# Kernel optimization log

Measured on AMD Instinct MI355X. Metric: run time of the kernel, lower is better.

Reference implementation:

```python
import jax, jax.numpy as jnp
import numpy as np

V = 8192
E = 262144
IN_DIM = 128
OUT_DIM = 128
NEG_SLOPE = 0.2


def setup_inputs() -> dict:
    key = jax.random.key(0)
    k1, k2, k3, k4 = jax.random.split(key, 4)
    h = jax.random.normal(k1, (V, IN_DIM), dtype=jnp.float32)
    edge_index = jax.random.randint(k2, (2, E), 0, V, dtype=jnp.int64)
    # nn.Linear weights: W (out_dim, in_dim), att (1, 2*out_dim), both bias-free
    W = jax.random.normal(k3, (OUT_DIM, IN_DIM), dtype=jnp.float32) / np.sqrt(IN_DIM)
    att_w = jax.random.normal(k4, (1, 2 * OUT_DIM), dtype=jnp.float32) / np.sqrt(2 * OUT_DIM)
    return {"h": h, "edge_index": edge_index, "W": W, "att_w": att_w}


def reference(h, edge_index, W, att_w):
    # h: (V, in_dim) -> (V, out_dim)
    hw = h @ W.T
    src, dst = edge_index[0], edge_index[1]
    # edge features: concat of endpoint embeddings -> (E, 2*out_dim)
    e = jnp.concatenate([hw[src], hw[dst]], axis=-1)
    # attention logits per edge, LeakyReLU(0.2)
    a = jax.nn.leaky_relu(jnp.squeeze(e @ att_w.T, -1), negative_slope=NEG_SLOPE)
    v = hw.shape[0]
    # faithful to original: dense V x V matrix, zeros on non-edges,
    # softmax over ALL columns (non-edges included as score 0)
    alpha = jnp.zeros((v, v), dtype=hw.dtype).at[src, dst].set(a)
    alpha = jax.nn.softmax(alpha, axis=-1)
    # dropout is identity in eval mode (deterministic reference)
    return alpha @ hw
```

## Files before the change

### kernel.cpp

```cpp
#include <hip/hip_runtime.h>
#include <hip/hip_bf16.h>
#include <math.h>


#define V 8192
#define E 262144
#define D 128
#define NEG_SLOPE 0.2f
#define CAP 96

__global__ __launch_bounds__(256) void k_hw(const float* __restrict__ h,
                                            const float* __restrict__ W,
                                            const float* __restrict__ att,
                                            float* __restrict__ hw,
                                            float* __restrict__ s1,
                                            float* __restrict__ s2,
                                            float* __restrict__ S) {
    __shared__ float Wt[D * 132];
    __shared__ float hs[8][D];
    __shared__ float atts[2 * D];
    for (int e = threadIdx.x; e < D * D; e += 256) {
        int o = e >> 7, k = e & 127;
        Wt[k * 132 + o] = W[e];
    }
    atts[threadIdx.x] = att[threadIdx.x];
    int c4 = (threadIdx.x & 31) * 4;
    int rsel = threadIdx.x >> 5;
    int rowbase = blockIdx.x * 32;
    float4 cs = make_float4(0.f, 0.f, 0.f, 0.f);
    for (int it = 0; it < 4; ++it) {
        int r0 = rowbase + it * 8;
        __syncthreads();
        for (int e = threadIdx.x; e < 8 * D; e += 256)
            hs[e >> 7][e & 127] = h[(r0 + (e >> 7)) * D + (e & 127)];
        __syncthreads();
        float a0 = 0.f, a1 = 0.f, a2 = 0.f, a3 = 0.f;
        const float* hrow = hs[rsel];
        #pragma unroll 8
        for (int k = 0; k < D; ++k) {
            float hk = hrow[k];
            float4 wv = *(const float4*)&Wt[k * 132 + c4];
            a0 += hk * wv.x; a1 += hk * wv.y; a2 += hk * wv.z; a3 += hk * wv.w;
        }
        int row = r0 + rsel;
        *(float4*)&hw[row * D + c4] = make_float4(a0, a1, a2, a3);
        cs.x += a0; cs.y += a1; cs.z += a2; cs.w += a3;
        float p1 = a0 * atts[c4] + a1 * atts[c4 + 1] + a2 * atts[c4 + 2] + a3 * atts[c4 + 3];
        float p2 = a0 * atts[D + c4] + a1 * atts[D + c4 + 1] + a2 * atts[D + c4 + 2] + a3 * atts[D + c4 + 3];
        #pragma unroll
        for (int m = 16; m; m >>= 1) {
            p1 += __shfl_xor(p1, m);
            p2 += __shfl_xor(p2, m);
        }
        if ((threadIdx.x & 31) == 0) { s1[row] = p1; s2[row] = p2; }
    }
    __syncthreads();
    hs[rsel][c4] = cs.x; hs[rsel][c4 + 1] = cs.y; hs[rsel][c4 + 2] = cs.z; hs[rsel][c4 + 3] = cs.w;
    __syncthreads();
    if (threadIdx.x < D) {
        float t = 0.f;
        #pragma unroll
        for (int r = 0; r < 8; ++r) t += hs[r][threadIdx.x];
        atomicAdd(&S[threadIdx.x], t);
    }
}

__global__ __launch_bounds__(256) void k_scatter(const int* __restrict__ ei,
                                                 const float* __restrict__ s1,
                                                 const float* __restrict__ s2,
                                                 int* __restrict__ cnt,
                                                 int2* __restrict__ bucket) {
    int e = blockIdx.x * 256 + threadIdx.x;
    int src = ei[e];
    int dst = ei[E + e];
    float a = s1[src] + s2[dst];
    a = a > 0.f ? a : NEG_SLOPE * a;
    float w = expf(a) - 1.f;
    int pos = atomicAdd(&cnt[src], 1);
    if (pos < CAP)
        bucket[src * CAP + pos] = make_int2(dst, __float_as_int(w));
}

__global__ __launch_bounds__(256) void k_row(const int2* __restrict__ bucket,
                                             const int* __restrict__ cnt,
                                             const float* __restrict__ hw,
                                             const float* __restrict__ S,
                                             float* __restrict__ out) {
    int row = (blockIdx.x * 256 + threadIdx.x) >> 6;
    int lane = threadIdx.x & 63;
    int deg = cnt[row];
    if (deg > CAP) deg = CAP;
    const int2* b = bucket + row * CAP;
    int2 e0 = b[lane];
    int2 e1 = (lane < CAP - 64) ? b[64 + lane] : make_int2(-1, 0);
    int d0 = e0.x; float w0 = __int_as_float(e0.y);
    int d1 = e1.x; float w1 = __int_as_float(e1.y);
    if (lane >= deg)      { d0 = -1; w0 = 0.f; }
    if (64 + lane >= deg) { d1 = -1; w1 = 0.f; }
    float2 acc = make_float2(0.f, 0.f);
    float dex = 0.f;
    int dmax0 = deg < 64 ? deg : 64;
    for (int j = 0; j < dmax0; ++j) {
        int   dj = __shfl(d0, j);
        float wj = __shfl(w0, j);
        bool dup = (d0 == dj) && (lane < j);
        if (__any(dup)) continue;
        float2 hv = *(const float2*)&hw[dj * D + lane * 2];
        acc.x += wj * hv.x; acc.y += wj * hv.y;
        dex += wj;
    }
    for (int j = 64; j < deg; ++j) {
        int   dj = __shfl(d1, j - 64);
        float wj = __shfl(w1, j - 64);
        bool dup = (d0 == dj) || ((d1 == dj) && (64 + lane < j));
        if (__any(dup)) continue;
        float2 hv = *(const float2*)&hw[dj * D + lane * 2];
        acc.x += wj * hv.x; acc.y += wj * hv.y;
        dex += wj;
    }
    float inv = 1.f / ((float)V + dex);
    float2 s = *(const float2*)&S[lane * 2];
    float2 o;
    o.x = (s.x + acc.x) * inv;
    o.y = (s.y + acc.y) * inv;
    *(float2*)&out[row * D + lane * 2] = o;
}

extern "C" void kernel_launch(void* const* d_in, const int* in_sizes, int n_in,
                              void* d_out, int out_size, void* d_ws, size_t ws_size,
                              hipStream_t stream) {
    const float* h   = (const float*)d_in[0];
    const int*   ei  = (const int*)d_in[1];
    const float* W   = (const float*)d_in[2];
    const float* att = (const float*)d_in[3];
    float* out = (float*)d_out;

    char* ws = (char*)d_ws;
    float* hw  = (float*)(ws);
    float* s1  = (float*)(ws + 4194304);
    float* s2  = (float*)(ws + 4227072);
    float* S   = (float*)(ws + 4259840);
    int*   cnt = (int*)(ws + 4260352);
    int2*  bucket = (int2*)(ws + 4293120);

    hipMemsetAsync(ws + 4259840, 0, 512 + 32768, stream);

    k_hw     <<<256,  256, 0, stream>>>(h, W, att, hw, s1, s2, S);
    k_scatter<<<1024, 256, 0, stream>>>(ei, s1, s2, cnt, bucket);
    k_row    <<<2048, 256, 0, stream>>>(bucket, cnt, hw, S, out);
}
```

Measured before the change: 117.8 us.

## Register-block hw GEMM, vectorize edge loads, precompute duplicate masks in row kernel

The projection kernel now gives each block 16 rows loaded once and has each thread compute two rows with float4 h reads, so every W tile read is reused and the per-iteration barriers are gone. The block count doubles to cover the rows. The scatter kernel handles four edges per thread using int4 loads of edge_index. The row kernel detects duplicate neighbours in a separate shuffle-only pass and zeros their weights, taking the warp vote and branch out of the gather loop. The cost is an extra O(deg) shuffle pass per row and more per-thread atomics in the scatter kernel.

```diff
diff --git a/kernel.cpp b/kernel.cpp
--- a/kernel.cpp
+++ b/kernel.cpp
@@ -9,6 +9,9 @@
 #define NEG_SLOPE 0.2f
 #define CAP 96
 
+#define FMA4(acc, hv, wv) { acc.x += (hv)*(wv).x; acc.y += (hv)*(wv).y; \
+                            acc.z += (hv)*(wv).z; acc.w += (hv)*(wv).w; }
+
 __global__ __launch_bounds__(256) void k_hw(const float* __restrict__ h,
                                             const float* __restrict__ W,
                                             const float* __restrict__ att,
@@ -17,50 +20,64 @@
                                             float* __restrict__ s2,
                                             float* __restrict__ S) {
     __shared__ float Wt[D * 132];
-    __shared__ float hs[8][D];
+    __shared__ float hs[16][D];
     __shared__ float atts[2 * D];
+    atts[threadIdx.x] = att[threadIdx.x];
     for (int e = threadIdx.x; e < D * D; e += 256) {
         int o = e >> 7, k = e & 127;
         Wt[k * 132 + o] = W[e];
     }
-    atts[threadIdx.x] = att[threadIdx.x];
+    int r0 = blockIdx.x * 16;
+    for (int e = threadIdx.x; e < 16 * D; e += 256)
+        hs[e >> 7][e & 127] = h[(r0 + (e >> 7)) * D + (e & 127)];
+    __syncthreads();
+
     int c4 = (threadIdx.x & 31) * 4;
-    int rsel = threadIdx.x >> 5;
-    int rowbase = blockIdx.x * 32;
-    float4 cs = make_float4(0.f, 0.f, 0.f, 0.f);
-    for (int it = 0; it < 4; ++it) {
-        int r0 = rowbase + it * 8;
-        __syncthreads();
-        for (int e = threadIdx.x; e < 8 * D; e += 256)
-            hs[e >> 7][e & 127] = h[(r0 + (e >> 7)) * D + (e & 127)];
-        __syncthreads();
-        float a0 = 0.f, a1 = 0.f, a2 = 0.f, a3 = 0.f;
-        const float* hrow = hs[rsel];
-        #pragma unroll 8
-        for (int k = 0; k < D; ++k) {
-            float hk = hrow[k];
-            float4 wv = *(const float4*)&Wt[k * 132 + c4];
-            a0 += hk * wv.x; a1 += hk * wv.y; a2 += hk * wv.z; a3 += hk * wv.w;
-        }
-        int row = r0 + rsel;
-        *(float4*)&hw[row * D + c4] = make_float4(a0, a1, a2, a3);
-        cs.x += a0; cs.y += a1; cs.z += a2; cs.w += a3;
-        float p1 = a0 * atts[c4] + a1 * atts[c4 + 1] + a2 * atts[c4 + 2] + a3 * atts[c4 + 3];
-        float p2 = a0 * atts[D + c4] + a1 * atts[D + c4 + 1] + a2 * atts[D + c4 + 2] + a3 * atts[D + c4 + 3];
-        #pragma unroll
-        for (int m = 16; m; m >>= 1) {
-            p1 += __shfl_xor(p1, m);
-            p2 += __shfl_xor(p2, m);
-        }
-        if ((threadIdx.x & 31) == 0) { s1[row] = p1; s2[row] = p2; }
+    int rq = threadIdx.x >> 5;
+    float4 acc0 = make_float4(0.f, 0.f, 0.f, 0.f);
+    float4 acc1 = make_float4(0.f, 0.f, 0.f, 0.f);
+    #pragma unroll 2
+    for (int kq = 0; kq < D; kq += 4) {
+        float4 ha = *(const float4*)&hs[rq][kq];
+        float4 hb = *(const float4*)&hs[rq + 8][kq];
+        float4 w0 = *(const float4*)&Wt[(kq + 0) * 132 + c4];
+        float4 w1 = *(const float4*)&Wt[(kq + 1) * 132 + c4];
+        float4 w2 = *(const float4*)&Wt[(kq + 2) * 132 + c4];
+        float4 w3 = *(const float4*)&Wt[(kq + 3) * 132 + c4];
+        FMA4(acc0, ha.x, w0); FMA4(acc0, ha.y, w1);
+        FMA4(acc0, ha.z, w2); FMA4(acc0, ha.w, w3);
+        FMA4(acc1, hb.x, w0); FMA4(acc1, hb.y, w1);
+        FMA4(acc1, hb.z, w2); FMA4(acc1, hb.w, w3);
     }
+    int rowa = r0 + rq, rowb = r0 + rq + 8;
+    *(float4*)&hw[rowa * D + c4] = acc0;
+    *(float4*)&hw[rowb * D + c4] = acc1;
+
+    float p1a = acc0.x * atts[c4] + acc0.y * atts[c4 + 1] + acc0.z * atts[c4 + 2] + acc0.w * atts[c4 + 3];
+    float p2a = acc0.x * atts[D + c4] + acc0.y * atts[D + c4 + 1] + acc0.z * atts[D + c4 + 2] + acc0.w * atts[D + c4 + 3];
+    float p1b = acc1.x * atts[c4] + acc1.y * atts[c4 + 1] + acc1.z * atts[c4 + 2] + acc1.w * atts[c4 + 3];
+    float p2b = acc1.x * atts[D + c4] + acc1.y * atts[D + c4 + 1] + acc1.z * atts[D + c4 + 2] + acc1.w * atts[D + c4 + 3];
+    #pragma unroll
+    for (int m = 16; m; m >>= 1) {
+        p1a += __shfl_xor(p1a, m); p2a += __shfl_xor(p2a, m);
+        p1b += __shfl_xor(p1b, m); p2b += __shfl_xor(p2b, m);
+    }
+    if ((threadIdx.x & 31) == 0) {
+        s1[rowa] = p1a; s2[rowa] = p2a;
+        s1[rowb] = p1b; s2[rowb] = p2b;
+    }
+
     __syncthreads();
-    hs[rsel][c4] = cs.x; hs[rsel][c4 + 1] = cs.y; hs[rsel][c4 + 2] = cs.z; hs[rsel][c4 + 3] = cs.w;
+    float* scr = &hs[0][0];
+    scr[rq * D + c4 + 0] = acc0.x + acc1.x;
+    scr[rq * D + c4 + 1] = acc0.y + acc1.y;
+    scr[rq * D + c4 + 2] = acc0.z + acc1.z;
+    scr[rq * D + c4 + 3] = acc0.w + acc1.w;
     __syncthreads();
     if (threadIdx.x < D) {
         float t = 0.f;
         #pragma unroll
-        for (int r = 0; r < 8; ++r) t += hs[r][threadIdx.x];
+        for (int r = 0; r < 8; ++r) t += scr[r * D + threadIdx.x];
         atomicAdd(&S[threadIdx.x], t);
     }
 }
@@ -70,15 +87,21 @@
                                                  const float* __restrict__ s2,
                                                  int* __restrict__ cnt,
                                                  int2* __restrict__ bucket) {
-    int e = blockIdx.x * 256 + threadIdx.x;
-    int src = ei[e];
-    int dst = ei[E + e];
-    float a = s1[src] + s2[dst];
-    a = a > 0.f ? a : NEG_SLOPE * a;
-    float w = expf(a) - 1.f;
-    int pos = atomicAdd(&cnt[src], 1);
-    if (pos < CAP)
-        bucket[src * CAP + pos] = make_int2(dst, __float_as_int(w));
+    int t = blockIdx.x * 256 + threadIdx.x;
+    int4 sv = *(const int4*)&ei[4 * t];
+    int4 dv = *(const int4*)&ei[E + 4 * t];
+    const int* sp = &sv.x;
+    const int* dp = &dv.x;
+    #pragma unroll
+    for (int j = 0; j < 4; ++j) {
+        int src = sp[j], dst = dp[j];
+        float a = s1[src] + s2[dst];
+        a = a > 0.f ? a : NEG_SLOPE * a;
+        float w = expf(a) - 1.f;
+        int pos = atomicAdd(&cnt[src], 1);
+        if (pos < CAP)
+            bucket[src * CAP + pos] = make_int2(dst, __float_as_int(w));
+    }
 }
 
 __global__ __launch_bounds__(256) void k_row(const int2* __restrict__ bucket,
@@ -93,18 +116,30 @@
     const int2* b = bucket + row * CAP;
     int2 e0 = b[lane];
     int2 e1 = (lane < CAP - 64) ? b[64 + lane] : make_int2(-1, 0);
-    int d0 = e0.x; float w0 = __int_as_float(e0.y);
-    int d1 = e1.x; float w1 = __int_as_float(e1.y);
-    if (lane >= deg)      { d0 = -1; w0 = 0.f; }
-    if (64 + lane >= deg) { d1 = -1; w1 = 0.f; }
+    int   d0 = (lane < deg)      ? e0.x : -1;
+    float w0 = (lane < deg)      ? __int_as_float(e0.y) : 0.f;
+    int   d1 = (64 + lane < deg) ? e1.x : -1;
+    float w1 = (64 + lane < deg) ? __int_as_float(e1.y) : 0.f;
+    int n0 = deg < 64 ? deg : 64;
+
+    bool dup0 = false, dup1 = false;
+    for (int j = 0; j < n0; ++j) {
+        int dj = __shfl(d0, j);
+        dup0 |= (d0 == dj) & (lane > j);
+        dup1 |= (d1 == dj);
+    }
+    for (int j = 64; j < deg; ++j) {
+        int dj = __shfl(d1, j - 64);
+        dup1 |= (d1 == dj) & (lane > j - 64);
+    }
+    if (dup0) w0 = 0.f;
+    if (dup1) w1 = 0.f;
+
     float2 acc = make_float2(0.f, 0.f);
     float dex = 0.f;
-    int dmax0 = deg < 64 ? deg : 64;
-    for (int j = 0; j < dmax0; ++j) {
+    for (int j = 0; j < n0; ++j) {
         int   dj = __shfl(d0, j);
         float wj = __shfl(w0, j);
-        bool dup = (d0 == dj) && (lane < j);
-        if (__any(dup)) continue;
         float2 hv = *(const float2*)&hw[dj * D + lane * 2];
         acc.x += wj * hv.x; acc.y += wj * hv.y;
         dex += wj;
@@ -112,12 +147,11 @@
     for (int j = 64; j < deg; ++j) {
         int   dj = __shfl(d1, j - 64);
         float wj = __shfl(w1, j - 64);
-        bool dup = (d0 == dj) || ((d1 == dj) && (64 + lane < j));
-        if (__any(dup)) continue;
         float2 hv = *(const float2*)&hw[dj * D + lane * 2];
         acc.x += wj * hv.x; acc.y += wj * hv.y;
         dex += wj;
     }
+
     float inv = 1.f / ((float)V + dex);
     float2 s = *(const float2*)&S[lane * 2];
     float2 o;
@@ -145,7 +179,7 @@
 
     hipMemsetAsync(ws + 4259840, 0, 512 + 32768, stream);
 
-    k_hw     <<<256,  256, 0, stream>>>(h, W, att, hw, s1, s2, S);
-    k_scatter<<<1024, 256, 0, stream>>>(ei, s1, s2, cnt, bucket);
+    k_hw     <<<512,  256, 0, stream>>>(h, W, att, hw, s1, s2, S);
+    k_scatter<<<256,  256, 0, stream>>>(ei, s1, s2, cnt, bucket);
     k_row    <<<2048, 256, 0, stream>>>(bucket, cnt, hw, S, out);
 }
```

Result: no change. 119.3 us (+1.3%).
